# Kernel tuning notes

Measured on AMD Instinct MI355X. Metric: run time of the kernel, lower is better.

## Reference

```python
import jax, jax.numpy as jnp
import numpy as np

B, T, D, H = 2, 4096, 768, 12
HD = D // H  # head_dim = 64


def setup_inputs() -> dict:
    key = jax.random.key(0)
    ks = jax.random.split(key, 6)
    s = 0.02
    return {
        "x": jax.random.normal(ks[0], (B, T, D), dtype=jnp.float32),
        "Wq": jax.random.normal(ks[1], (D, D), dtype=jnp.float32) * s,
        "Wk": jax.random.normal(ks[2], (D, D), dtype=jnp.float32) * s,
        "Wv": jax.random.normal(ks[3], (D, D), dtype=jnp.float32) * s,
        "Wo": jax.random.normal(ks[4], (D, D), dtype=jnp.float32) * s,
        "bo": jnp.zeros((D,), dtype=jnp.float32),
    }


def reference(x, Wq, Wk, Wv, Wo, bo):
    b, t, d = x.shape
    # QKV projections (no bias), reshape to [B, H, T, HD]
    def heads(w):
        return (x @ w.T).reshape(b, t, H, HD).transpose(0, 2, 1, 3)
    q, k, v = heads(Wq), heads(Wk), heads(Wv)
    scores = jnp.einsum("bhqd,bhkd->bhqk", q, k)  # [B,H,T,T]
    causal = jnp.tril(jnp.ones((t, t), dtype=bool))
    scores = jnp.where(causal, scores, -jnp.inf)
    attn = jax.nn.softmax(scores / jnp.sqrt(jnp.float32(HD)), axis=-1)
    ctx = jnp.einsum("bhqk,bhkd->bhqd", attn, v)  # [B,H,T,HD]
    ctx = ctx.transpose(0, 2, 1, 3).reshape(b, t, d)
    return ctx @ Wo.T + bo
```

## Files before the change

kernel.cpp:

```cpp
#include <hip/hip_runtime.h>
#include <hip/hip_bf16.h>
#include <cstdint>
#include <cstddef>

#define B_  2
#define T_  4096
#define D_  768
#define H_  12
#define HD_ 64
#define M_  (B_*T_)

#define SCL 0.18033688f

typedef __bf16 bf16x8 __attribute__((ext_vector_type(8)));
typedef float  f32x4  __attribute__((ext_vector_type(4)));
typedef short  s16x4  __attribute__((ext_vector_type(4)));
using bf16 = __hip_bfloat16;

__device__ inline float fexp2(float x) {
  float r; asm("v_exp_f32 %0, %1" : "=v"(r) : "v"(x)); return r;
}
__device__ inline uint32_t fu(float x) { union { float f; uint32_t u; } c; c.f = x; return c.u; }
__device__ inline uint32_t pktr(float a, float b) {
  return __builtin_amdgcn_perm(fu(b), fu(a), 0x07060302);
}
__device__ inline f32x4 mfma16(s16x4 a, s16x4 b, f32x4 c) {
#if __has_builtin(__builtin_amdgcn_mfma_f32_16x16x16bf16_1k)
  return __builtin_amdgcn_mfma_f32_16x16x16bf16_1k(a, b, c, 0, 0, 0);
#else
  asm("v_mfma_f32_16x16x16_bf16 %0, %1, %2, %0" : "+v"(c) : "v"(a), "v"(b));
  return c;
#endif
}
#define GLD16(g, l) __builtin_amdgcn_global_load_lds( \
    (const __attribute__((address_space(1))) uint32_t*)(const void*)(g), \
    (__attribute__((address_space(3))) uint32_t*)(void*)(l), 16, 0, 0)

__global__ void cvt_all(const float* __restrict__ x,
                        const float* __restrict__ w0, const float* __restrict__ w1,
                        const float* __restrict__ w2, const float* __restrict__ w3,
                        bf16* __restrict__ xd,
                        bf16* __restrict__ d0, bf16* __restrict__ d1,
                        bf16* __restrict__ d2, bf16* __restrict__ d3) {
  int blk = blockIdx.x;
  const float* s; bf16* d; int i;
  if (blk < 6144) {
    s = x; d = xd; i = blk * 256 + threadIdx.x;
  } else {
    int q = blk - 6144, which = q / 576, rb = q % 576;
    switch (which) {
      case 0: s = w0; d = d0; break;
      case 1: s = w1; d = d1; break;
      case 2: s = w2; d = d2; break;
      default: s = w3; d = d3; break;
    }
    i = rb * 256 + threadIdx.x;
  }
  float4 v = ((const float4*)s)[i];
  union { bf16 o[4]; uint2 u; } pk;
  pk.o[0] = __float2bfloat16(v.x); pk.o[1] = __float2bfloat16(v.y);
  pk.o[2] = __float2bfloat16(v.z); pk.o[3] = __float2bfloat16(v.w);
  *(uint2*)(d + 4 * (size_t)i) = pk.u;
}

__global__ __launch_bounds__(256) void gemm_qkv(const bf16* __restrict__ x,
                                                const bf16* __restrict__ W0,
                                                const bf16* __restrict__ W1,
                                                const bf16* __restrict__ W2,
                                                bf16* __restrict__ O0,
                                                bf16* __restrict__ O1,
                                                bf16* __restrict__ O2t) {
  __shared__ bf16 As[2][4096];
  __shared__ bf16 Bs[2][4096];
  const int flat = blockIdx.x;
  const int by = flat / 18;
  const int rr = flat % 18;
  const int z  = rr / 6;
  const int bx = rr % 6;
  const bf16* Wz = (z == 0) ? W0 : ((z == 1) ? W1 : W2);
  const char* Ap; const char* Bp; int a0, b0;
  if (z == 2) { Ap = (const char*)x;  a0 = by * 128; Bp = (const char*)Wz; b0 = bx * 128; }
  else        { Ap = (const char*)Wz; a0 = bx * 128; Bp = (const char*)x;  b0 = by * 128; }
  const int t = threadIdx.x;
  const int w = t >> 6, lane = t & 63;
  const int wa = (w >> 1) * 64, wb = (w & 1) * 64;
  const int mi = lane & 15, qd = lane >> 4;

  int aoff[2], boff[2];
  #pragma unroll
  for (int i = 0; i < 2; ++i) {
    int L = i * 256 + t;
    int row = L >> 2, sl = L & 3, c = sl ^ (row & 3);
    aoff[i] = (a0 + row) * 1536 + c * 16;
    boff[i] = (b0 + row) * 1536 + c * 16;
  }
  const int fsw = (qd ^ (mi & 3)) * 8;

  f32x4 acc[4][4] = {};

  #pragma unroll
  for (int i = 0; i < 2; ++i) {
    GLD16(Ap + aoff[i], &As[0][i * 2048 + w * 512]);
    GLD16(Bp + boff[i], &Bs[0][i * 2048 + w * 512]);
  }

  for (int kk = 0; kk < 24; ++kk) {
    __syncthreads();
    const int par = kk & 1;
    if (kk + 1 < 24) {
      const int np = par ^ 1, kb = (kk + 1) * 64;
      #pragma unroll
      for (int i = 0; i < 2; ++i) {
        GLD16(Ap + aoff[i] + kb, &As[np][i * 2048 + w * 512]);
        GLD16(Bp + boff[i] + kb, &Bs[np][i * 2048 + w * 512]);
      }
    }
    bf16x8 af[4], bfr[4];
    #pragma unroll
    for (int at = 0; at < 4; ++at)
      af[at] = *(const bf16x8*)&As[par][(wa + at * 16 + mi) * 32 + fsw];
    #pragma unroll
    for (int bt = 0; bt < 4; ++bt)
      bfr[bt] = *(const bf16x8*)&Bs[par][(wb + bt * 16 + mi) * 32 + fsw];
    #pragma unroll
    for (int at = 0; at < 4; ++at)
      #pragma unroll
      for (int bt = 0; bt < 4; ++bt)
        acc[at][bt] = __builtin_amdgcn_mfma_f32_16x16x32_bf16(af[at], bfr[bt], acc[at][bt], 0, 0, 0);
  }

  if (z == 2) {
    #pragma unroll
    for (int at = 0; at < 4; ++at)
      #pragma unroll
      for (int bt = 0; bt < 4; ++bt) {
        int gr = a0 + wa + at * 16 + qd * 4;
        int gc = b0 + wb + bt * 16 + mi;
        union { bf16 o[4]; uint2 u; } pk;
        #pragma unroll
        for (int r = 0; r < 4; ++r) pk.o[r] = __float2bfloat16(acc[at][bt][r]);
        int bb = gr >> 12, tt = gr & 4095;
        int ttw = tt ^ (((gc >> 3) & 1) << 2);
        *(uint2*)(O2t + (size_t)bb * 768 * 4096 + (size_t)gc * 4096 + ttw) = pk.u;
      }
  } else {
    const float scl = (z == 1) ? SCL : 1.0f;
    bf16* Ob = (z == 0) ? O0 : O1;
    #pragma unroll
    for (int at = 0; at < 4; ++at)
      #pragma unroll
      for (int bt = 0; bt < 4; ++bt) {
        int f0  = a0 + wa + at * 16 + qd * 4;
        int tkn = b0 + wb + bt * 16 + mi;
        union { bf16 o[4]; uint2 u; } pk;
        #pragma unroll
        for (int r = 0; r < 4; ++r) pk.o[r] = __float2bfloat16(acc[at][bt][r] * scl);
        *(uint2*)(Ob + (size_t)tkn * 768 + f0) = pk.u;
      }
  }
}

__global__ __launch_bounds__(256) void gemm_out(const bf16* __restrict__ ctx,
                                                const bf16* __restrict__ Wo,
                                                float* __restrict__ Cf,
                                                const float* __restrict__ bias) {
  __shared__ bf16 As[2][4096];
  __shared__ bf16 Bs[2][4096];
  const int flat = blockIdx.x;
  const int by = flat / 6, bx = flat % 6;
  const char* Ap = (const char*)Wo;  const int a0 = bx * 128;
  const char* Bp = (const char*)ctx; const int b0 = by * 128;
  const int t = threadIdx.x;
  const int w = t >> 6, lane = t & 63;
  const int wa = (w >> 1) * 64, wb = (w & 1) * 64;
  const int mi = lane & 15, qd = lane >> 4;

  int aoff[2], boff[2];
  #pragma unroll
  for (int i = 0; i < 2; ++i) {
    int L = i * 256 + t;
    int row = L >> 2, sl = L & 3, c = sl ^ (row & 3);
    aoff[i] = (a0 + row) * 1536 + c * 16;
    boff[i] = (b0 + row) * 1536 + c * 16;
  }
  const int fsw = (qd ^ (mi & 3)) * 8;

  f32x4 acc[4][4] = {};

  #pragma unroll
  for (int i = 0; i < 2; ++i) {
    GLD16(Ap + aoff[i], &As[0][i * 2048 + w * 512]);
    GLD16(Bp + boff[i], &Bs[0][i * 2048 + w * 512]);
  }

  for (int kk = 0; kk < 24; ++kk) {
    __syncthreads();
    const int par = kk & 1;
    if (kk + 1 < 24) {
      const int np = par ^ 1, kb = (kk + 1) * 64;
      #pragma unroll
      for (int i = 0; i < 2; ++i) {
        GLD16(Ap + aoff[i] + kb, &As[np][i * 2048 + w * 512]);
        GLD16(Bp + boff[i] + kb, &Bs[np][i * 2048 + w * 512]);
      }
    }
    bf16x8 af[4], bfr[4];
    #pragma unroll
    for (int at = 0; at < 4; ++at)
      af[at] = *(const bf16x8*)&As[par][(wa + at * 16 + mi) * 32 + fsw];
    #pragma unroll
    for (int bt = 0; bt < 4; ++bt)
      bfr[bt] = *(const bf16x8*)&Bs[par][(wb + bt * 16 + mi) * 32 + fsw];
    #pragma unroll
    for (int at = 0; at < 4; ++at)
      #pragma unroll
      for (int bt = 0; bt < 4; ++bt)
        acc[at][bt] = __builtin_amdgcn_mfma_f32_16x16x32_bf16(af[at], bfr[bt], acc[at][bt], 0, 0, 0);
  }

  #pragma unroll
  for (int at = 0; at < 4; ++at)
    #pragma unroll
    for (int bt = 0; bt < 4; ++bt) {
      int f0  = a0 + wa + at * 16 + qd * 4;
      int tkn = b0 + wb + bt * 16 + mi;
      float4 bv = *(const float4*)&bias[f0];
      float4 o;
      o.x = acc[at][bt][0] + bv.x; o.y = acc[at][bt][1] + bv.y;
      o.z = acc[at][bt][2] + bv.z; o.w = acc[at][bt][3] + bv.w;
      *(float4*)&Cf[(size_t)tkn * 768 + f0] = o;
    }
}

__global__ __launch_bounds__(256, 5) void flash_attn(const bf16* __restrict__ Q,
                                                     const bf16* __restrict__ K,
                                                     const bf16* __restrict__ Vt,
                                                     bf16* __restrict__ ctx) {
  __shared__ bf16 Ks[2][4096];
  __shared__ bf16 Vs[2][4096];
  const int t = threadIdx.x;
  const int w = t >> 6, lane = t & 63;
  const int mi = lane & 15, qd = lane >> 4;
  const int bh   = blockIdx.x % 24;
  const int qrev = blockIdx.x / 24;
  const int q0 = T_ - 64 - qrev * 64;
  const int b = bh / H_, h = bh % H_;
  const size_t bTD = (size_t)b * T_ * D_;
  const char* Kp = (const char*)(K  + bTD + (size_t)h * HD_);
  const char* Vp = (const char*)(Vt + (size_t)b * D_ * T_ + (size_t)h * HD_ * T_);
  const int qw = q0 + w * 16;

  int vkoff[2], vvoff[2];
  #pragma unroll
  for (int i = 0; i < 2; ++i) {
    int L = i * 256 + t;
    int rl = L >> 3, c = (L & 7) ^ (rl & 7);
    vkoff[i] = rl * 1536 + c * 16;
    vvoff[i] = rl * 8192 + c * 16;
  }

  int fidx[4][2];
  #pragma unroll
  for (int jt = 0; jt < 4; ++jt)
    #pragma unroll
    for (int kt = 0; kt < 2; ++kt)
      fidx[jt][kt] = (jt * 16 + mi) * 64 + (((kt * 4 + qd) ^ (mi & 7)) * 8);

  int vbase[4];
  #pragma unroll
  for (int ks = 0; ks < 4; ++ks)
    vbase[ks] = (((2 * ks + (qd >> 1)) ^ (mi & 7)) * 8) +
                (((qd & 1) ^ ((mi >> 3) & 1)) * 4) + mi * 64;

  bf16x8 qf[2];
  const bf16* Qp = Q + bTD + (size_t)h * HD_;
  #pragma unroll
  for (int kt = 0; kt < 2; ++kt)
    qf[kt] = *(const bf16x8*)(Qp + (size_t)(qw + mi) * D_ + kt * 32 + qd * 8);

  f32x4 oacc[4] = {};
  float lst = 0.f;
  const int ntiles = q0 / 64 + 1;

  #pragma unroll
  for (int i = 0; i < 2; ++i) {
    GLD16(Kp + vkoff[i], &Ks[0][i * 2048 + w * 512]);
    GLD16(Vp + vvoff[i], &Vs[0][i * 2048 + w * 512]);
  }

  for (int tt = 0; tt < ntiles; ++tt) {
    __syncthreads();
    const int par = tt & 1;
    if (tt + 1 < ntiles) {
      const size_t j1 = (size_t)(tt + 1) * 64;
      const int np = par ^ 1;
      #pragma unroll
      for (int i = 0; i < 2; ++i) {
        GLD16(Kp + vkoff[i] + j1 * 1536, &Ks[np][i * 2048 + w * 512]);
        GLD16(Vp + vvoff[i] + j1 * 2,    &Vs[np][i * 2048 + w * 512]);
      }
    }
    const int j0 = tt * 64;

    f32x4 sacc[4] = {};
    #pragma unroll
    for (int jt = 0; jt < 4; ++jt)
      #pragma unroll
      for (int kt = 0; kt < 2; ++kt) {
        bf16x8 kf = *(const bf16x8*)&Ks[par][fidx[jt][kt]];
        sacc[jt] = __builtin_amdgcn_mfma_f32_16x16x32_bf16(kf, qf[kt], sacc[jt], 0, 0, 0);
      }

    if (j0 + 63 > qw) {
      const int qg = qw + mi;
      #pragma unroll
      for (int jt = 0; jt < 4; ++jt)
        #pragma unroll
        for (int r = 0; r < 4; ++r) {
          int jg = j0 + jt * 16 + qd * 4 + r;
          if (jg > qg) sacc[jt][r] = -1e30f;
        }
    }

    s16x4 pB[4];
    #pragma unroll
    for (int jt = 0; jt < 4; ++jt) {
      float p0 = fexp2(sacc[jt][0]);
      float p1 = fexp2(sacc[jt][1]);
      float p2 = fexp2(sacc[jt][2]);
      float p3 = fexp2(sacc[jt][3]);
      lst += (p0 + p1) + (p2 + p3);
      union { uint32_t u[2]; s16x4 s; } pw;
      pw.u[0] = pktr(p0, p1);
      pw.u[1] = pktr(p2, p3);
      pB[jt] = pw.s;
    }

    #pragma unroll
    for (int ks = 0; ks < 4; ++ks)
      #pragma unroll
      for (int dt = 0; dt < 4; ++dt) {
        s16x4 vf = *(const s16x4*)&Vs[par][vbase[ks] + dt * 1024];
        oacc[dt] = mfma16(vf, pB[ks], oacc[dt]);
      }
  }

  float l = lst;
  l += __shfl_xor(l, 16);
  l += __shfl_xor(l, 32);
  float inv = __builtin_amdgcn_rcpf(l);
  const int qg = qw + mi;
  bf16* cp = ctx + bTD + (size_t)qg * D_ + h * HD_ + qd * 4;
  #pragma unroll
  for (int dt = 0; dt < 4; ++dt) {
    union { bf16 o[4]; uint2 u; } pko;
    #pragma unroll
    for (int r = 0; r < 4; ++r) pko.o[r] = __float2bfloat16(oacc[dt][r] * inv);
    *(uint2*)(cp + dt * 16) = pko.u;
  }
}

extern "C" void kernel_launch(void* const* d_in, const int* in_sizes, int n_in,
                              void* d_out, int out_size, void* d_ws, size_t ws_size,
                              hipStream_t stream) {
  const float* x  = (const float*)d_in[0];
  const float* Wq = (const float*)d_in[1];
  const float* Wk = (const float*)d_in[2];
  const float* Wv = (const float*)d_in[3];
  const float* Wo = (const float*)d_in[4];
  const float* bo = (const float*)d_in[5];
  float* out = (float*)d_out;

  char* ws = (char*)d_ws;
  const size_t SZ  = (size_t)M_ * D_ * 2;
  const size_t WSZ = (size_t)D_ * D_ * 2;
  bf16* xb   = (bf16*)(ws);
  bf16* Qb   = (bf16*)(ws + 1 * SZ);
  bf16* Kb   = (bf16*)(ws + 2 * SZ);
  bf16* Vtg  = (bf16*)(ws + 3 * SZ);
  bf16* ctxb = (bf16*)(ws + 4 * SZ);
  bf16* Wqb  = (bf16*)(ws + 5 * SZ);
  bf16* Wkb  = (bf16*)(ws + 5 * SZ + 1 * WSZ);
  bf16* Wvb  = (bf16*)(ws + 5 * SZ + 2 * WSZ);
  bf16* Wob  = (bf16*)(ws + 5 * SZ + 3 * WSZ);

  cvt_all<<<6144 + 4 * 576, 256, 0, stream>>>(x, Wq, Wk, Wv, Wo, xb, Wqb, Wkb, Wvb, Wob);

  gemm_qkv<<<1152, 256, 0, stream>>>(xb, Wqb, Wkb, Wvb, Qb, Kb, Vtg);

  flash_attn<<<(T_ / 64) * B_ * H_, 256, 0, stream>>>(Qb, Kb, Vtg, ctxb);

  gemm_out<<<384, 256, 0, stream>>>(ctxb, Wob, out, bo);
}
```

Baseline: 242.0 us.

## Double flash-attention query tile per wave and halve output GEMM tile width

Flash attention now processes 128 queries per block (32 per wave, two 16-row subtiles) so each K/V tile loaded into LDS feeds twice as many MFMAs. Tiles past a wave's causal range are skipped per wave, and s_setprio brackets the MFMA phases. Occupancy hint drops from 5 to 3 to allow the extra accumulators. The output GEMM switches to 64x128 tiles with 768 blocks, giving more blocks to fill the CUs at the cost of less reuse per block. The larger attention blocks also mean fewer blocks and more uneven causal work, which may hurt load balance.

```diff
diff --git a/kernel.cpp b/kernel.cpp
--- a/kernel.cpp
+++ b/kernel.cpp
@@ -164,62 +164,61 @@
                                                 const bf16* __restrict__ Wo,
                                                 float* __restrict__ Cf,
                                                 const float* __restrict__ bias) {
-  __shared__ bf16 As[2][4096];
+  __shared__ bf16 As[2][2048];
   __shared__ bf16 Bs[2][4096];
   const int flat = blockIdx.x;
-  const int by = flat / 6, bx = flat % 6;
-  const char* Ap = (const char*)Wo;  const int a0 = bx * 128;
+  const int by = flat / 12, bx = flat % 12;
+  const char* Ap = (const char*)Wo;  const int a0 = bx * 64;
   const char* Bp = (const char*)ctx; const int b0 = by * 128;
   const int t = threadIdx.x;
   const int w = t >> 6, lane = t & 63;
-  const int wa = (w >> 1) * 64, wb = (w & 1) * 64;
+  const int wa = (w >> 1) * 32, wb = (w & 1) * 64;
   const int mi = lane & 15, qd = lane >> 4;
 
-  int aoff[2], boff[2];
+  int aoff, boff[2];
+  { int row = t >> 2, sl = t & 3, c = sl ^ (row & 3);
+    aoff = (a0 + row) * 1536 + c * 16; }
   #pragma unroll
   for (int i = 0; i < 2; ++i) {
     int L = i * 256 + t;
     int row = L >> 2, sl = L & 3, c = sl ^ (row & 3);
-    aoff[i] = (a0 + row) * 1536 + c * 16;
     boff[i] = (b0 + row) * 1536 + c * 16;
   }
   const int fsw = (qd ^ (mi & 3)) * 8;
 
-  f32x4 acc[4][4] = {};
-
-  #pragma unroll
-  for (int i = 0; i < 2; ++i) {
-    GLD16(Ap + aoff[i], &As[0][i * 2048 + w * 512]);
+  f32x4 acc[2][4] = {};
+
+  GLD16(Ap + aoff, &As[0][w * 512]);
+  #pragma unroll
+  for (int i = 0; i < 2; ++i)
     GLD16(Bp + boff[i], &Bs[0][i * 2048 + w * 512]);
-  }
 
   for (int kk = 0; kk < 24; ++kk) {
     __syncthreads();
     const int par = kk & 1;
     if (kk + 1 < 24) {
       const int np = par ^ 1, kb = (kk + 1) * 64;
-      #pragma unroll
-      for (int i = 0; i < 2; ++i) {
-        GLD16(Ap + aoff[i] + kb, &As[np][i * 2048 + w * 512]);
+      GLD16(Ap + aoff + kb, &As[np][w * 512]);
+      #pragma unroll
+      for (int i = 0; i < 2; ++i)
         GLD16(Bp + boff[i] + kb, &Bs[np][i * 2048 + w * 512]);
-      }
-    }
-    bf16x8 af[4], bfr[4];
-    #pragma unroll
-    for (int at = 0; at < 4; ++at)
+    }
+    bf16x8 af[2], bfr[4];
+    #pragma unroll
+    for (int at = 0; at < 2; ++at)
       af[at] = *(const bf16x8*)&As[par][(wa + at * 16 + mi) * 32 + fsw];
     #pragma unroll
     for (int bt = 0; bt < 4; ++bt)
       bfr[bt] = *(const bf16x8*)&Bs[par][(wb + bt * 16 + mi) * 32 + fsw];
     #pragma unroll
-    for (int at = 0; at < 4; ++at)
+    for (int at = 0; at < 2; ++at)
       #pragma unroll
       for (int bt = 0; bt < 4; ++bt)
         acc[at][bt] = __builtin_amdgcn_mfma_f32_16x16x32_bf16(af[at], bfr[bt], acc[at][bt], 0, 0, 0);
   }
 
   #pragma unroll
-  for (int at = 0; at < 4; ++at)
+  for (int at = 0; at < 2; ++at)
     #pragma unroll
     for (int bt = 0; bt < 4; ++bt) {
       int f0  = a0 + wa + at * 16 + qd * 4;
@@ -232,7 +231,7 @@
     }
 }
 
-__global__ __launch_bounds__(256, 5) void flash_attn(const bf16* __restrict__ Q,
+__global__ __launch_bounds__(256, 3) void flash_attn(const bf16* __restrict__ Q,
                                                      const bf16* __restrict__ K,
                                                      const bf16* __restrict__ Vt,
                                                      bf16* __restrict__ ctx) {
@@ -243,12 +242,12 @@
   const int mi = lane & 15, qd = lane >> 4;
   const int bh   = blockIdx.x % 24;
   const int qrev = blockIdx.x / 24;
-  const int q0 = T_ - 64 - qrev * 64;
+  const int q0 = T_ - 128 - qrev * 128;
   const int b = bh / H_, h = bh % H_;
   const size_t bTD = (size_t)b * T_ * D_;
   const char* Kp = (const char*)(K  + bTD + (size_t)h * HD_);
   const char* Vp = (const char*)(Vt + (size_t)b * D_ * T_ + (size_t)h * HD_ * T_);
-  const int qw = q0 + w * 16;
+  const int qw = q0 + w * 32;
 
   int vkoff[2], vvoff[2];
   #pragma unroll
@@ -272,15 +271,17 @@
     vbase[ks] = (((2 * ks + (qd >> 1)) ^ (mi & 7)) * 8) +
                 (((qd & 1) ^ ((mi >> 3) & 1)) * 4) + mi * 64;
 
-  bf16x8 qf[2];
+  bf16x8 qf[2][2];
   const bf16* Qp = Q + bTD + (size_t)h * HD_;
   #pragma unroll
-  for (int kt = 0; kt < 2; ++kt)
-    qf[kt] = *(const bf16x8*)(Qp + (size_t)(qw + mi) * D_ + kt * 32 + qd * 8);
-
-  f32x4 oacc[4] = {};
-  float lst = 0.f;
-  const int ntiles = q0 / 64 + 1;
+  for (int s = 0; s < 2; ++s)
+    #pragma unroll
+    for (int kt = 0; kt < 2; ++kt)
+      qf[s][kt] = *(const bf16x8*)(Qp + (size_t)(qw + s * 16 + mi) * D_ + kt * 32 + qd * 8);
+
+  f32x4 oacc[2][4] = {};
+  float lst[2] = {0.f, 0.f};
+  const int ntiles = q0 / 64 + 2;
 
   #pragma unroll
   for (int i = 0; i < 2; ++i) {
@@ -301,62 +302,77 @@
       }
     }
     const int j0 = tt * 64;
-
-    f32x4 sacc[4] = {};
+    if (j0 > qw + 31) continue;
+
+    f32x4 sacc[2][4] = {};
+    __builtin_amdgcn_s_setprio(1);
     #pragma unroll
     for (int jt = 0; jt < 4; ++jt)
       #pragma unroll
       for (int kt = 0; kt < 2; ++kt) {
         bf16x8 kf = *(const bf16x8*)&Ks[par][fidx[jt][kt]];
-        sacc[jt] = __builtin_amdgcn_mfma_f32_16x16x32_bf16(kf, qf[kt], sacc[jt], 0, 0, 0);
-      }
+        sacc[0][jt] = __builtin_amdgcn_mfma_f32_16x16x32_bf16(kf, qf[0][kt], sacc[0][jt], 0, 0, 0);
+        sacc[1][jt] = __builtin_amdgcn_mfma_f32_16x16x32_bf16(kf, qf[1][kt], sacc[1][jt], 0, 0, 0);
+      }
+    __builtin_amdgcn_s_setprio(0);
 
     if (j0 + 63 > qw) {
-      const int qg = qw + mi;
-      #pragma unroll
-      for (int jt = 0; jt < 4; ++jt)
+      #pragma unroll
+      for (int s = 0; s < 2; ++s) {
+        const int qg = qw + s * 16 + mi;
         #pragma unroll
-        for (int r = 0; r < 4; ++r) {
-          int jg = j0 + jt * 16 + qd * 4 + r;
-          if (jg > qg) sacc[jt][r] = -1e30f;
-        }
-    }
-
-    s16x4 pB[4];
-    #pragma unroll
-    for (int jt = 0; jt < 4; ++jt) {
-      float p0 = fexp2(sacc[jt][0]);
-      float p1 = fexp2(sacc[jt][1]);
-      float p2 = fexp2(sacc[jt][2]);
-      float p3 = fexp2(sacc[jt][3]);
-      lst += (p0 + p1) + (p2 + p3);
-      union { uint32_t u[2]; s16x4 s; } pw;
-      pw.u[0] = pktr(p0, p1);
-      pw.u[1] = pktr(p2, p3);
-      pB[jt] = pw.s;
-    }
-
+        for (int jt = 0; jt < 4; ++jt)
+          #pragma unroll
+          for (int r = 0; r < 4; ++r) {
+            int jg = j0 + jt * 16 + qd * 4 + r;
+            if (jg > qg) sacc[s][jt][r] = -1e30f;
+          }
+      }
+    }
+
+    s16x4 pB[2][4];
+    #pragma unroll
+    for (int s = 0; s < 2; ++s)
+      #pragma unroll
+      for (int jt = 0; jt < 4; ++jt) {
+        float p0 = fexp2(sacc[s][jt][0]);
+        float p1 = fexp2(sacc[s][jt][1]);
+        float p2 = fexp2(sacc[s][jt][2]);
+        float p3 = fexp2(sacc[s][jt][3]);
+        lst[s] += (p0 + p1) + (p2 + p3);
+        union { uint32_t u[2]; s16x4 v; } pw;
+        pw.u[0] = pktr(p0, p1);
+        pw.u[1] = pktr(p2, p3);
+        pB[s][jt] = pw.v;
+      }
+
+    __builtin_amdgcn_s_setprio(1);
     #pragma unroll
     for (int ks = 0; ks < 4; ++ks)
       #pragma unroll
       for (int dt = 0; dt < 4; ++dt) {
         s16x4 vf = *(const s16x4*)&Vs[par][vbase[ks] + dt * 1024];
-        oacc[dt] = mfma16(vf, pB[ks], oacc[dt]);
-      }
-  }
-
-  float l = lst;
-  l += __shfl_xor(l, 16);
-  l += __shfl_xor(l, 32);
-  float inv = __builtin_amdgcn_rcpf(l);
-  const int qg = qw + mi;
-  bf16* cp = ctx + bTD + (size_t)qg * D_ + h * HD_ + qd * 4;
-  #pragma unroll
-  for (int dt = 0; dt < 4; ++dt) {
-    union { bf16 o[4]; uint2 u; } pko;
-    #pragma unroll
-    for (int r = 0; r < 4; ++r) pko.o[r] = __float2bfloat16(oacc[dt][r] * inv);
-    *(uint2*)(cp + dt * 16) = pko.u;
+        oacc[0][dt] = mfma16(vf, pB[0][ks], oacc[0][dt]);
+        oacc[1][dt] = mfma16(vf, pB[1][ks], oacc[1][dt]);
+      }
+    __builtin_amdgcn_s_setprio(0);
+  }
+
+  #pragma unroll
+  for (int s = 0; s < 2; ++s) {
+    float l = lst[s];
+    l += __shfl_xor(l, 16);
+    l += __shfl_xor(l, 32);
+    float inv = __builtin_amdgcn_rcpf(l);
+    const int qg = qw + s * 16 + mi;
+    bf16* cp = ctx + bTD + (size_t)qg * D_ + h * HD_ + qd * 4;
+    #pragma unroll
+    for (int dt = 0; dt < 4; ++dt) {
+      union { bf16 o[4]; uint2 u; } pko;
+      #pragma unroll
+      for (int r = 0; r < 4; ++r) pko.o[r] = __float2bfloat16(oacc[s][dt][r] * inv);
+      *(uint2*)(cp + dt * 16) = pko.u;
+    }
   }
 }
 
@@ -388,7 +404,7 @@
 
   gemm_qkv<<<1152, 256, 0, stream>>>(xb, Wqb, Wkb, Wvb, Qb, Kb, Vtg);
 
-  flash_attn<<<(T_ / 64) * B_ * H_, 256, 0, stream>>>(Qb, Kb, Vtg, ctxb);
-
-  gemm_out<<<384, 256, 0, stream>>>(ctxb, Wob, out, bo);
-}
+  flash_attn<<<(T_ / 128) * B_ * H_, 256, 0, stream>>>(Qb, Kb, Vtg, ctxb);
+
+  gemm_out<<<768, 256, 0, stream>>>(ctxb, Wob, out, bo);
+}
```

Measured after the change: 254.7 us. 1.05x slower.
